# Performance work log

Hardware: AMD Instinct MI355X
Metric: run time of the kernel (lower is better)

Reference implementation:

```python
import jax, jax.numpy as jnp
import numpy as np

N = 100000
E = 1600000
IN_CH = 128
HID = 32
HEADS = 8
OUT_CH = 40
NEG_SLOPE = 0.2


def _glorot(key, shape):
    fan = shape[0] + shape[-1]
    return jax.random.normal(key, shape, dtype=jnp.float32) * jnp.sqrt(2.0 / fan)


def gat_conv(x, src, dst, W, att_src, att_dst, bias, heads, out_ch, concat):
    # PyG GATConv (eval mode, dropout inactive, self-loops already appended)
    n = x.shape[0]
    h = (x @ W).reshape(n, heads, out_ch)              # [N,H,C]
    a_s = jnp.sum(h * att_src, axis=-1)                # [N,H]
    a_d = jnp.sum(h * att_dst, axis=-1)                # [N,H]
    e = jax.nn.leaky_relu(a_s[src] + a_d[dst], NEG_SLOPE)  # [E,H]
    # softmax over incoming edges of each destination node
    m = jax.ops.segment_max(e, dst, num_segments=n)
    e = jnp.exp(e - m[dst])
    denom = jax.ops.segment_sum(e, dst, num_segments=n)
    alpha = e / denom[dst]                              # [E,H]
    msg = h[src] * alpha[:, :, None]                    # [E,H,C] gather + weight
    out = jax.ops.segment_sum(msg, dst, num_segments=n)  # [N,H,C] scatter-add
    if concat:
        out = out.reshape(n, heads * out_ch)
    else:
        out = out.mean(axis=1)
    return out + bias


def setup_inputs() -> dict:
    key = jax.random.key(0)
    ks = jax.random.split(key, 16)
    x = jax.random.normal(ks[0], (N, IN_CH), dtype=jnp.float32)
    edge_index = jax.random.randint(ks[1], (2, E), 0, N, dtype=jnp.int64)
    params = {
        "W1": _glorot(ks[2], (IN_CH, HEADS * HID)),
        "as1": _glorot(ks[3], (HEADS, HID)),
        "ad1": _glorot(ks[4], (HEADS, HID)),
        "b1": jnp.zeros((HEADS * HID,), jnp.float32),
        "W2": _glorot(ks[5], (HEADS * HID, HID)),
        "as2": _glorot(ks[6], (1, HID)),
        "ad2": _glorot(ks[7], (1, HID)),
        "b2": jnp.zeros((HID,), jnp.float32),
        "W3": _glorot(ks[8], (HID, OUT_CH)),
        "as3": _glorot(ks[9], (1, OUT_CH)),
        "ad3": _glorot(ks[10], (1, OUT_CH)),
        "b3": jnp.zeros((OUT_CH,), jnp.float32),
    }
    return {"x": x, "edge_index": edge_index, **params}


def reference(x, edge_index, W1, as1, ad1, b1, W2, as2, ad2, b2, W3, as3, ad3, b3):
    n = x.shape[0]
    # PyG GATConv adds self-loops by default
    loops = jnp.arange(n, dtype=edge_index.dtype)
    src = jnp.concatenate([edge_index[0], loops])
    dst = jnp.concatenate([edge_index[1], loops])

    h = gat_conv(x, src, dst, W1, as1, ad1, b1, HEADS, HID, concat=True)
    h = jax.nn.elu(h)
    h = gat_conv(h, src, dst, W2, as2, ad2, b2, 1, HID, concat=False)
    h = jax.nn.elu(h)
    h = gat_conv(h, src, dst, W3, as3, ad3, b3, 1, OUT_CH, concat=False)
    return jax.nn.log_softmax(h, axis=1)
```

## Files before the change

kernel.cpp:

```cpp
#include <hip/hip_runtime.h>

#define NN 100000
#define NE 1600000
#define ET 1700000
#define NEG 0.2f
#define FNEG 3.4e38f
#define NBSC 98
#define GEMM1_NB 1563
#define PE_NB 6641
#define FATA_NB 8305
#define FILL_CH 425000

#define SRC_OFF   0ULL
#define DST_OFF   6800000ULL
#define RP_OFF    13600000ULL
#define CSR_OFF   14400128ULL
#define W1F_OFF   21200128ULL
#define W2F_OFF   21265664ULL
#define W3F_OFF   21282048ULL
#define SC_OFF    21285120ULL
#define H_OFF     21286144ULL
#define H2B_OFF   72486144ULL
#define H3B_OFF   88486144ULL
#define ALPH_OFF  123686144ULL
#define ASN_OFF   150886144ULL
#define ADN_OFF   154086144ULL
#define AS2_OFF   157286144ULL
#define AD2_OFF   157686144ULL
#define CNT8_OFF  158086144ULL
#define RANK_OFF  161286144ULL
#define WS_NEED   168086144ULL

typedef short bf16x8 __attribute__((ext_vector_type(8)));
typedef float f32x4 __attribute__((ext_vector_type(4)));
typedef float f32x2 __attribute__((ext_vector_type(2)));

__device__ __forceinline__ float lrelu(float x) { return x > 0.f ? x : NEG * x; }
__device__ __forceinline__ float b2f(unsigned short u) {
  return __uint_as_float(((unsigned)u) << 16);
}
__device__ __forceinline__ unsigned short f2bu(float f) {
  unsigned u = __float_as_uint(f);
  return (unsigned short)((u + 0x7FFFu + ((u >> 16) & 1u)) >> 16);
}

__global__ __launch_bounds__(256) void k_sentinel(float* out, int n) {
  int i = blockIdx.x * 256 + threadIdx.x;
  if (i < n) out[i] = 12345.0f;
}

__global__ __launch_bounds__(256) void k_prep_w(const float* __restrict__ W1,
                                                const float* __restrict__ W2,
                                                const float* __restrict__ W3,
                                                unsigned short* __restrict__ W1f,
                                                unsigned short* __restrict__ W2f,
                                                unsigned short* __restrict__ W3f) {
  int idx = blockIdx.x * 256 + threadIdx.x;
  if (idx < 4096) {
    int fg = idx >> 6, lane = idx & 63;
    int mf = fg >> 2, kk = fg & 3;
    int c = mf * 16 + (lane & 15), k0 = kk * 32 + (lane >> 4) * 8;
    unsigned short* o = W1f + idx * 8;
    #pragma unroll
    for (int j = 0; j < 8; ++j) o[j] = f2bu(W1[(k0 + j) * 256 + c]);
  } else if (idx < 5120) {
    int t = idx - 4096;
    int fg = t >> 6, lane = t & 63;
    int mf = fg >> 3, kk = fg & 7;
    int c = mf * 16 + (lane & 15), k0 = kk * 32 + (lane >> 4) * 8;
    unsigned short* o = W2f + t * 8;
    #pragma unroll
    for (int j = 0; j < 8; ++j) o[j] = f2bu(W2[(k0 + j) * 32 + c]);
  } else if (idx < 5312) {
    int t = idx - 5120;
    int mf = t >> 6, lane = t & 63;
    int c = mf * 16 + (lane & 15), k0 = (lane >> 4) * 8;
    unsigned short* o = W3f + t * 8;
    #pragma unroll
    for (int j = 0; j < 8; ++j) o[j] = (c < 40) ? f2bu(W3[(k0 + j) * 40 + c]) : 0;
  }
}

__global__ __launch_bounds__(256) void k_fatA(const int* __restrict__ raw,
                                              int* __restrict__ src,
                                              int* __restrict__ dst,
                                              int* __restrict__ cnt8,
                                              int* __restrict__ rank,
                                              const float* __restrict__ x,
                                              const bf16x8* __restrict__ W1f,
                                              const float* __restrict__ as1,
                                              const float* __restrict__ ad1,
                                              unsigned char* __restrict__ h8,
                                              float* __restrict__ a_s,
                                              float* __restrict__ a_d) {
  __shared__ __align__(16) unsigned short xs[64 * 128];
  __shared__ float asL[256], adL[256];
  const int bid = blockIdx.x;
  const int grp = bid / 5, rem = bid - grp * 5;
  const int tid = threadIdx.x;

  if (rem != 4) {
    int pe = grp * 4 + rem;
    if (pe >= PE_NB) return;
    bool is64 = true;
    #pragma unroll
    for (int i = 1; i < 32; i += 2) is64 = is64 && (raw[i] == 0);
    long long e = (long long)pe * 256 + tid;
    if (e >= ET) return;
    int s, d;
    if (e < NE) {
      if (is64) {
        const long long* r = (const long long*)raw;
        s = (int)r[e];
        d = (int)r[NE + e];
      } else {
        s = raw[e];
        d = raw[NE + e];
      }
    } else {
      s = d = (int)(e - NE);
    }
    src[e] = s;
    dst[e] = d;
    rank[e] = atomicAdd(&cnt8[(tid & 7) * NN + d], 1);
    return;
  }

  if (grp >= GEMM1_NB) return;
  const int n0 = grp * 64;
  asL[tid] = as1[tid];
  adL[tid] = ad1[tid];
  for (int j = tid; j < 2048; j += 256) {
    int r = j >> 5;
    int c4 = (j & 31) << 2;
    long long row = n0 + r; if (row >= NN) row = NN - 1;
    float4 v = *(const float4*)(x + row * 128 + c4);
    unsigned short* p = &xs[r * 128 + c4];
    p[0] = f2bu(v.x); p[1] = f2bu(v.y); p[2] = f2bu(v.z); p[3] = f2bu(v.w);
  }
  __syncthreads();
  const int w = tid >> 6, lane = tid & 63;
  const int nloc = w * 16 + (lane & 15);
  const int node = n0 + nloc;
  bf16x8 bfr[4];
  #pragma unroll
  for (int kk = 0; kk < 4; ++kk)
    bfr[kk] = *(const bf16x8*)&xs[nloc * 128 + kk * 32 + (lane >> 4) * 8];
  const int ch_base = (lane >> 4) * 4;
  float sA[8] = {}, sD[8] = {};
  #pragma unroll
  for (int mf = 0; mf < 16; ++mf) {
    f32x4 acc = {0.f, 0.f, 0.f, 0.f};
    #pragma unroll
    for (int kk = 0; kk < 4; ++kk) {
      bf16x8 af = W1f[(mf * 4 + kk) * 64 + lane];
      acc = __builtin_amdgcn_mfma_f32_16x16x32_bf16(af, bfr[kk], acc, 0, 0, 0);
    }
    const float* av = &asL[mf * 16 + ch_base];
    const float* dv = &adL[mf * 16 + ch_base];
    float ps = acc[0] * av[0] + acc[1] * av[1] + acc[2] * av[2] + acc[3] * av[3];
    float pd = acc[0] * dv[0] + acc[1] * dv[1] + acc[2] * dv[2] + acc[3] * dv[3];
    ps += __shfl_xor(ps, 16); ps += __shfl_xor(ps, 32);
    pd += __shfl_xor(pd, 16); pd += __shfl_xor(pd, 32);
    sA[mf >> 1] += ps; sD[mf >> 1] += pd;
    if (node < NN) {
      int w01 = __builtin_amdgcn_cvt_pk_fp8_f32(acc[0], acc[1], 0, false);
      int w0123 = __builtin_amdgcn_cvt_pk_fp8_f32(acc[2], acc[3], w01, true);
      *(unsigned*)&h8[(unsigned)(node * 256 + mf * 16 + ch_base)] = (unsigned)w0123;
    }
  }
  if (lane < 16 && node < NN) {
    #pragma unroll
    for (int hd = 0; hd < 8; ++hd) {
      a_s[node * 8 + hd] = sA[hd];
      a_d[node * 8 + hd] = sD[hd];
    }
  }
}

__global__ __launch_bounds__(1024) void k_scan_a(int* __restrict__ cnt8,
                                                 int* __restrict__ rowptr,
                                                 int* __restrict__ bsum) {
  __shared__ int wsum[16];
  const int lane = threadIdx.x & 63, wid = threadIdx.x >> 6;
  int i = blockIdx.x * 1024 + threadIdx.x;
  int x = 0;
  if (i < NN) {
    int run = 0;
    #pragma unroll
    for (int k = 0; k < 8; ++k) {
      int c = cnt8[k * NN + i];
      cnt8[k * NN + i] = run;
      run += c;
    }
    x = run;
  }
  int inc = x;
  #pragma unroll
  for (int off = 1; off < 64; off <<= 1) {
    int t = __shfl_up(inc, off);
    if (lane >= off) inc += t;
  }
  if (lane == 63) wsum[wid] = inc;
  __syncthreads();
  if (wid == 0) {
    int w = (lane < 16) ? wsum[lane] : 0;
    #pragma unroll
    for (int off = 1; off < 16; off <<= 1) {
      int t = __shfl_up(w, off);
      if (lane >= off) w += t;
    }
    if (lane < 16) wsum[lane] = w;
  }
  __syncthreads();
  int base = wid ? wsum[wid - 1] : 0;
  if (i < NN) rowptr[i + 1] = base + inc;
  if (threadIdx.x == 1023) bsum[blockIdx.x] = base + inc;
}

__global__ __launch_bounds__(128) void k_scan_b(int* __restrict__ bsum) {
  __shared__ int w0tot;
  int tid = threadIdx.x;
  int v = (tid < NBSC) ? bsum[tid] : 0;
  int inc = v;
  #pragma unroll
  for (int off = 1; off < 64; off <<= 1) {
    int t = __shfl_up(inc, off);
    if ((tid & 63) >= off) inc += t;
  }
  if (tid == 63) w0tot = inc;
  __syncthreads();
  if (tid >= 64) inc += w0tot;
  if (tid < NBSC) bsum[tid] = inc - v;
}

__global__ __launch_bounds__(1024) void k_scan_c(int* __restrict__ rowptr,
                                                 const int* __restrict__ bsum) {
  int i = blockIdx.x * 1024 + threadIdx.x;
  if (i < NN) rowptr[i + 1] += bsum[blockIdx.x];
  if (i == 0) rowptr[0] = 0;
}

__global__ __launch_bounds__(256) void k_fill_nr(const int* __restrict__ src,
                                                 const int* __restrict__ dst,
                                                 const int* __restrict__ rank,
                                                 const int* __restrict__ cnt8,
                                                 const int* __restrict__ rowptr,
                                                 int* __restrict__ csr) {
  int gid = blockIdx.x * 256 + threadIdx.x;
  if (gid >= FILL_CH) return;
  const int h = gid & 7;
  int e0 = gid, e1 = gid + FILL_CH, e2 = gid + 2 * FILL_CH, e3 = gid + 3 * FILL_CH;
  int d0 = dst[e0], d1 = dst[e1], d2 = dst[e2], d3 = dst[e3];
  int r0 = rank[e0], r1 = rank[e1], r2 = rank[e2], r3 = rank[e3];
  int s0 = src[e0], s1 = src[e1], s2 = src[e2], s3 = src[e3];
  int p0 = cnt8[h * NN + d0], p1 = cnt8[h * NN + d1];
  int p2 = cnt8[h * NN + d2], p3 = cnt8[h * NN + d3];
  int b0 = rowptr[d0], b1 = rowptr[d1], b2 = rowptr[d2], b3 = rowptr[d3];
  csr[b0 + p0 + r0] = s0;
  csr[b1 + p1 + r1] = s1;
  csr[b2 + p2 + r2] = s2;
  csr[b3 + p3 + r3] = s3;
}

__global__ __launch_bounds__(256) void k_msalpha1(const int* __restrict__ rowptr,
                                                  const int* __restrict__ csr,
                                                  const float* __restrict__ a_s,
                                                  const float* __restrict__ a_d,
                                                  unsigned short* __restrict__ alph) {
  const int node = blockIdx.x * 4 + (threadIdx.x >> 6);
  const int lane = threadIdx.x & 63;
  const int beg = __builtin_amdgcn_readfirstlane(rowptr[node]);
  const int end = __builtin_amdgcn_readfirstlane(rowptr[node + 1]);
  const int hd = lane & 7;
  const int eg = lane >> 3;
  const float adv = a_d[node * 8 + hd];
  float mx = -FNEG, sm = 0.f;
  if (end - beg <= 32) {
    float vc0 = 0.f, vc1 = 0.f, vc2 = 0.f, vc3 = 0.f;
    #pragma unroll
    for (int k = 0; k < 4; ++k) {
      int i = beg + eg + k * 8;
      if (i < end) {
        float v = lrelu(a_s[csr[i] * 8 + hd] + adv);
        if (k == 0) vc0 = v; else if (k == 1) vc1 = v;
        else if (k == 2) vc2 = v; else vc3 = v;
        float nm = fmaxf(mx, v);
        sm = sm * __expf(mx - nm) + __expf(v - nm);
        mx = nm;
      }
    }
    #pragma unroll
    for (int off = 8; off < 64; off <<= 1) {
      float mo = __shfl_xor(mx, off);
      float so = __shfl_xor(sm, off);
      float nm = fmaxf(mx, mo);
      sm = sm * __expf(mx - nm) + so * __expf(mo - nm);
      mx = nm;
    }
    float rden = 1.0f / sm;
    #pragma unroll
    for (int k = 0; k < 4; ++k) {
      int i = beg + eg + k * 8;
      if (i < end) {
        float v = (k == 0) ? vc0 : (k == 1) ? vc1 : (k == 2) ? vc2 : vc3;
        alph[i * 8 + hd] = f2bu(__expf(v - mx) * rden);
      }
    }
  } else {
    for (int i = beg + eg; i < end; i += 8) {
      int s = csr[i];
      float v = lrelu(a_s[s * 8 + hd] + adv);
      float nm = fmaxf(mx, v);
      sm = sm * __expf(mx - nm) + __expf(v - nm);
      mx = nm;
    }
    #pragma unroll
    for (int off = 8; off < 64; off <<= 1) {
      float mo = __shfl_xor(mx, off);
      float so = __shfl_xor(sm, off);
      float nm = fmaxf(mx, mo);
      sm = sm * __expf(mx - nm) + so * __expf(mo - nm);
      mx = nm;
    }
    float rden = 1.0f / sm;
    for (int i = beg + eg; i < end; i += 8) {
      int s = csr[i];
      float v = lrelu(a_s[s * 8 + hd] + adv);
      alph[i * 8 + hd] = f2bu(__expf(v - mx) * rden);
    }
  }
}

__global__ __launch_bounds__(1024) void k_gather1f(const int* __restrict__ rowptr,
                                                   const int* __restrict__ csr,
                                                   const unsigned short* __restrict__ alph,
                                                   const unsigned char* __restrict__ h8,
                                                   const float* __restrict__ b,
                                                   const bf16x8* __restrict__ W2f,
                                                   const float* __restrict__ as2,
                                                   const float* __restrict__ ad2,
                                                   unsigned short* __restrict__ h2,
                                                   float* __restrict__ a_s,
                                                   float* __restrict__ a_d) {
  __shared__ __align__(16) unsigned short xs[16 * 256];
  const int tid = threadIdx.x;
  const int w = tid >> 6, lane = tid & 63;
  const int n0 = blockIdx.x * 16;
  const int node = n0 + w;
  const int beg = __builtin_amdgcn_readfirstlane(rowptr[node]);
  const int end = __builtin_amdgcn_readfirstlane(rowptr[node + 1]);
  const int hd2 = lane >> 3;
  const unsigned l4 = lane * 4;
  float4 acc = {0.f, 0.f, 0.f, 0.f};
  int i = beg;
  for (; i + 8 <= end; i += 8) {
    int s0 = __builtin_amdgcn_readfirstlane(csr[i]);
    int s1 = __builtin_amdgcn_readfirstlane(csr[i + 1]);
    int s2 = __builtin_amdgcn_readfirstlane(csr[i + 2]);
    int s3 = __builtin_amdgcn_readfirstlane(csr[i + 3]);
    int s4 = __builtin_amdgcn_readfirstlane(csr[i + 4]);
    int s5 = __builtin_amdgcn_readfirstlane(csr[i + 5]);
    int s6 = __builtin_amdgcn_readfirstlane(csr[i + 6]);
    int s7 = __builtin_amdgcn_readfirstlane(csr[i + 7]);
    float a0 = b2f(alph[(i + 0) * 8 + hd2]);
    float a1 = b2f(alph[(i + 1) * 8 + hd2]);
    float a2 = b2f(alph[(i + 2) * 8 + hd2]);
    float a3 = b2f(alph[(i + 3) * 8 + hd2]);
    float a4 = b2f(alph[(i + 4) * 8 + hd2]);
    float a5 = b2f(alph[(i + 5) * 8 + hd2]);
    float a6 = b2f(alph[(i + 6) * 8 + hd2]);
    float a7 = b2f(alph[(i + 7) * 8 + hd2]);
    unsigned w0 = *(const unsigned*)(h8 + ((unsigned)(s0 << 8) + l4));
    unsigned w1 = *(const unsigned*)(h8 + ((unsigned)(s1 << 8) + l4));
    unsigned w2 = *(const unsigned*)(h8 + ((unsigned)(s2 << 8) + l4));
    unsigned w3 = *(const unsigned*)(h8 + ((unsigned)(s3 << 8) + l4));
    unsigned w4 = *(const unsigned*)(h8 + ((unsigned)(s4 << 8) + l4));
    unsigned w5 = *(const unsigned*)(h8 + ((unsigned)(s5 << 8) + l4));
    unsigned w6 = *(const unsigned*)(h8 + ((unsigned)(s6 << 8) + l4));
    unsigned w7 = *(const unsigned*)(h8 + ((unsigned)(s7 << 8) + l4));
    f32x2 lo, hi;
    lo = __builtin_amdgcn_cvt_pk_f32_fp8(w0, false); hi = __builtin_amdgcn_cvt_pk_f32_fp8(w0, true);
    acc.x += a0 * lo[0]; acc.y += a0 * lo[1]; acc.z += a0 * hi[0]; acc.w += a0 * hi[1];
    lo = __builtin_amdgcn_cvt_pk_f32_fp8(w1, false); hi = __builtin_amdgcn_cvt_pk_f32_fp8(w1, true);
    acc.x += a1 * lo[0]; acc.y += a1 * lo[1]; acc.z += a1 * hi[0]; acc.w += a1 * hi[1];
    lo = __builtin_amdgcn_cvt_pk_f32_fp8(w2, false); hi = __builtin_amdgcn_cvt_pk_f32_fp8(w2, true);
    acc.x += a2 * lo[0]; acc.y += a2 * lo[1]; acc.z += a2 * hi[0]; acc.w += a2 * hi[1];
    lo = __builtin_amdgcn_cvt_pk_f32_fp8(w3, false); hi = __builtin_amdgcn_cvt_pk_f32_fp8(w3, true);
    acc.x += a3 * lo[0]; acc.y += a3 * lo[1]; acc.z += a3 * hi[0]; acc.w += a3 * hi[1];
    lo = __builtin_amdgcn_cvt_pk_f32_fp8(w4, false); hi = __builtin_amdgcn_cvt_pk_f32_fp8(w4, true);
    acc.x += a4 * lo[0]; acc.y += a4 * lo[1]; acc.z += a4 * hi[0]; acc.w += a4 * hi[1];
    lo = __builtin_amdgcn_cvt_pk_f32_fp8(w5, false); hi = __builtin_amdgcn_cvt_pk_f32_fp8(w5, true);
    acc.x += a5 * lo[0]; acc.y += a5 * lo[1]; acc.z += a5 * hi[0]; acc.w += a5 * hi[1];
    lo = __builtin_amdgcn_cvt_pk_f32_fp8(w6, false); hi = __builtin_amdgcn_cvt_pk_f32_fp8(w6, true);
    acc.x += a6 * lo[0]; acc.y += a6 * lo[1]; acc.z += a6 * hi[0]; acc.w += a6 * hi[1];
    lo = __builtin_amdgcn_cvt_pk_f32_fp8(w7, false); hi = __builtin_amdgcn_cvt_pk_f32_fp8(w7, true);
    acc.x += a7 * lo[0]; acc.y += a7 * lo[1]; acc.z += a7 * hi[0]; acc.w += a7 * hi[1];
  }
  for (; i < end; ++i) {
    int s0 = __builtin_amdgcn_readfirstlane(csr[i]);
    float a0 = b2f(alph[i * 8 + hd2]);
    unsigned w0 = *(const unsigned*)(h8 + ((unsigned)(s0 << 8) + l4));
    f32x2 lo = __builtin_amdgcn_cvt_pk_f32_fp8(w0, false);
    f32x2 hi = __builtin_amdgcn_cvt_pk_f32_fp8(w0, true);
    acc.x += a0 * lo[0]; acc.y += a0 * lo[1]; acc.z += a0 * hi[0]; acc.w += a0 * hi[1];
  }
  float4 bv = *(const float4*)(b + l4);
  acc.x += bv.x; acc.y += bv.y; acc.z += bv.z; acc.w += bv.w;
  acc.x = acc.x > 0.f ? acc.x : expm1f(acc.x);
  acc.y = acc.y > 0.f ? acc.y : expm1f(acc.y);
  acc.z = acc.z > 0.f ? acc.z : expm1f(acc.z);
  acc.w = acc.w > 0.f ? acc.w : expm1f(acc.w);
  {
    ushort4 o;
    o.x = f2bu(acc.x); o.y = f2bu(acc.y); o.z = f2bu(acc.z); o.w = f2bu(acc.w);
    *(ushort4*)&xs[w * 256 + l4] = o;
  }
  __syncthreads();
  if (w == 0) {
    const int nloc = lane & 15;
    const int node2 = n0 + nloc;
    const int ch_base = (lane >> 4) * 4;
    float sA = 0.f, sD = 0.f;
    #pragma unroll
    for (int mf = 0; mf < 2; ++mf) {
      f32x4 c2 = {0.f, 0.f, 0.f, 0.f};
      #pragma unroll
      for (int kk = 0; kk < 8; ++kk) {
        bf16x8 bfr = *(const bf16x8*)&xs[nloc * 256 + kk * 32 + (lane >> 4) * 8];
        c2 = __builtin_amdgcn_mfma_f32_16x16x32_bf16(W2f[(mf * 8 + kk) * 64 + lane],
                                                     bfr, c2, 0, 0, 0);
      }
      float4 av = *(const float4*)(as2 + mf * 16 + ch_base);
      float4 dv = *(const float4*)(ad2 + mf * 16 + ch_base);
      float ps = c2[0] * av.x + c2[1] * av.y + c2[2] * av.z + c2[3] * av.w;
      float pd = c2[0] * dv.x + c2[1] * dv.y + c2[2] * dv.z + c2[3] * dv.w;
      ps += __shfl_xor(ps, 16); ps += __shfl_xor(ps, 32);
      pd += __shfl_xor(pd, 16); pd += __shfl_xor(pd, 32);
      sA += ps; sD += pd;
      ushort4 o;
      o.x = f2bu(c2[0]); o.y = f2bu(c2[1]); o.z = f2bu(c2[2]); o.w = f2bu(c2[3]);
      *(ushort4*)&h2[(unsigned)(node2 * 32 + mf * 16 + ch_base)] = o;
    }
    if (lane < 16) { a_s[node2] = sA; a_d[node2] = sD; }
  }
}

__global__ __launch_bounds__(512) void k_gather2f(const int* __restrict__ rowptr,
                                                  const int* __restrict__ csr,
                                                  const float* __restrict__ a_s,
                                                  const float* __restrict__ a_d,
                                                  const unsigned short* __restrict__ h,
                                                  const float* __restrict__ b,
                                                  const bf16x8* __restrict__ W3f,
                                                  const float* __restrict__ as3,
                                                  const float* __restrict__ ad3,
                                                  unsigned short* __restrict__ h3,
                                                  float* __restrict__ a_s3,
                                                  float* __restrict__ a_d3) {
  __shared__ __align__(16) unsigned short xs[16 * 32];
  const int tid = threadIdx.x;
  const int hw = tid >> 5, lane32 = tid & 31;
  const int n0 = blockIdx.x * 16;
  const int node = n0 + hw;
  const int beg = rowptr[node], end = rowptr[node + 1];
  const float adv = a_d[node];

  float mx = -FNEG, sm = 0.f;
  for (int i = beg + lane32; i < end; i += 32) {
    float v = lrelu(a_s[csr[i]] + adv);
    float nm = fmaxf(mx, v);
    sm = sm * __expf(mx - nm) + __expf(v - nm);
    mx = nm;
  }
  #pragma unroll
  for (int off = 1; off < 32; off <<= 1) {
    float mo = __shfl_xor(mx, off, 32);
    float so = __shfl_xor(sm, off, 32);
    float nm = fmaxf(mx, mo);
    sm = sm * __expf(mx - nm) + so * __expf(mo - nm);
    mx = nm;
  }
  float rden = 1.0f / sm;

  float acc = 0.f;
  int i = beg;
  for (; i + 4 <= end; i += 4) {
    int s0 = csr[i], s1 = csr[i + 1], s2 = csr[i + 2], s3 = csr[i + 3];
    float a0 = __expf(lrelu(a_s[s0] + adv) - mx) * rden;
    float a1 = __expf(lrelu(a_s[s1] + adv) - mx) * rden;
    float a2 = __expf(lrelu(a_s[s2] + adv) - mx) * rden;
    float a3 = __expf(lrelu(a_s[s3] + adv) - mx) * rden;
    unsigned short v0 = h[(unsigned)(s0 * 32 + lane32)];
    unsigned short v1 = h[(unsigned)(s1 * 32 + lane32)];
    unsigned short v2 = h[(unsigned)(s2 * 32 + lane32)];
    unsigned short v3 = h[(unsigned)(s3 * 32 + lane32)];
    acc += a0 * b2f(v0) + a1 * b2f(v1) + a2 * b2f(v2) + a3 * b2f(v3);
  }
  for (; i < end; ++i) {
    int s0 = csr[i];
    float a0 = __expf(lrelu(a_s[s0] + adv) - mx) * rden;
    acc += a0 * b2f(h[(unsigned)(s0 * 32 + lane32)]);
  }
  acc += b[lane32];
  acc = acc > 0.f ? acc : expm1f(acc);
  xs[hw * 32 + lane32] = f2bu(acc);
  __syncthreads();
  if (tid < 64) {
    const int lane = tid;
    const int nloc = lane & 15;
    const int node3 = n0 + nloc;
    const int ch_base = (lane >> 4) * 4;
    bf16x8 bfr = *(const bf16x8*)&xs[nloc * 32 + (lane >> 4) * 8];
    float sA = 0.f, sD = 0.f;
    #pragma unroll
    for (int mf = 0; mf < 3; ++mf) {
      f32x4 c3 = {0.f, 0.f, 0.f, 0.f};
      c3 = __builtin_amdgcn_mfma_f32_16x16x32_bf16(W3f[mf * 64 + lane], bfr, c3, 0, 0, 0);
      int ch0 = mf * 16 + ch_base;
      float4 av = {0.f, 0.f, 0.f, 0.f}, dv = {0.f, 0.f, 0.f, 0.f};
      if (ch0 < 40) {
        av = *(const float4*)(as3 + ch0);
        dv = *(const float4*)(ad3 + ch0);
      }
      float ps = c3[0] * av.x + c3[1] * av.y + c3[2] * av.z + c3[3] * av.w;
      float pd = c3[0] * dv.x + c3[1] * dv.y + c3[2] * dv.z + c3[3] * dv.w;
      ps += __shfl_xor(ps, 16); ps += __shfl_xor(ps, 32);
      pd += __shfl_xor(pd, 16); pd += __shfl_xor(pd, 32);
      sA += ps; sD += pd;
      if (ch0 < 40) {
        ushort4 o;
        o.x = f2bu(c3[0]); o.y = f2bu(c3[1]); o.z = f2bu(c3[2]); o.w = f2bu(c3[3]);
        *(ushort4*)&h3[(unsigned)(node3 * 40 + ch0)] = o;
      }
    }
    if (lane < 16) { a_s3[node3] = sA; a_d3[node3] = sD; }
  }
}

__global__ __launch_bounds__(256) void k_gather3f(const int* __restrict__ rowptr,
                                                  const int* __restrict__ csr,
                                                  const float* __restrict__ a_s,
                                                  const float* __restrict__ a_d,
                                                  const unsigned short* __restrict__ h,
                                                  const float* __restrict__ b,
                                                  float* __restrict__ out) {
  const int node = blockIdx.x * 4 + (threadIdx.x >> 6);
  const int lane = threadIdx.x & 63;
  const int beg = __builtin_amdgcn_readfirstlane(rowptr[node]);
  const int end = __builtin_amdgcn_readfirstlane(rowptr[node + 1]);
  const float adv = a_d[node];

  float mx = -FNEG, sm = 0.f;
  for (int i = beg + lane; i < end; i += 64) {
    float v = lrelu(a_s[csr[i]] + adv);
    float nm = fmaxf(mx, v);
    sm = sm * __expf(mx - nm) + __expf(v - nm);
    mx = nm;
  }
  #pragma unroll
  for (int off = 1; off < 64; off <<= 1) {
    float mo = __shfl_xor(mx, off);
    float so = __shfl_xor(sm, off);
    float nm = fmaxf(mx, mo);
    sm = sm * __expf(mx - nm) + so * __expf(mo - nm);
    mx = nm;
  }
  float rden = 1.0f / sm;

  float acc = 0.f;
  int i = beg;
  for (; i + 4 <= end; i += 4) {
    int s0 = __builtin_amdgcn_readfirstlane(csr[i]);
    int s1 = __builtin_amdgcn_readfirstlane(csr[i + 1]);
    int s2 = __builtin_amdgcn_readfirstlane(csr[i + 2]);
    int s3 = __builtin_amdgcn_readfirstlane(csr[i + 3]);
    float a0 = __expf(lrelu(a_s[s0] + adv) - mx) * rden;
    float a1 = __expf(lrelu(a_s[s1] + adv) - mx) * rden;
    float a2 = __expf(lrelu(a_s[s2] + adv) - mx) * rden;
    float a3 = __expf(lrelu(a_s[s3] + adv) - mx) * rden;
    if (lane < 40) {
      unsigned short v0 = h[(unsigned)(s0 * 40 + lane)];
      unsigned short v1 = h[(unsigned)(s1 * 40 + lane)];
      unsigned short v2 = h[(unsigned)(s2 * 40 + lane)];
      unsigned short v3 = h[(unsigned)(s3 * 40 + lane)];
      acc += a0 * b2f(v0) + a1 * b2f(v1) + a2 * b2f(v2) + a3 * b2f(v3);
    }
  }
  for (; i < end; ++i) {
    int s0 = __builtin_amdgcn_readfirstlane(csr[i]);
    float a0 = __expf(lrelu(a_s[s0] + adv) - mx) * rden;
    if (lane < 40) acc += a0 * b2f(h[(unsigned)(s0 * 40 + lane)]);
  }
  float v = (lane < 40) ? acc + b[lane] : -FNEG;
  float vmax = v;
  #pragma unroll
  for (int off = 1; off < 64; off <<= 1) vmax = fmaxf(vmax, __shfl_xor(vmax, off));
  float ex = (lane < 40) ? __expf(v - vmax) : 0.f;
  float es = ex;
  #pragma unroll
  for (int off = 1; off < 64; off <<= 1) es += __shfl_xor(es, off);
  float lse = vmax + __logf(es);
  if (lane < 40) out[(long long)node * 40 + lane] = v - lse;
}

extern "C" void kernel_launch(void* const* d_in, const int* in_sizes, int n_in,
                              void* d_out, int out_size, void* d_ws, size_t ws_size,
                              hipStream_t stream) {
  const float* x   = (const float*)d_in[0];
  const int*   eix = (const int*)d_in[1];
  const float* W1  = (const float*)d_in[2];
  const float* as1 = (const float*)d_in[3];
  const float* ad1 = (const float*)d_in[4];
  const float* b1  = (const float*)d_in[5];
  const float* W2  = (const float*)d_in[6];
  const float* as2 = (const float*)d_in[7];
  const float* ad2 = (const float*)d_in[8];
  const float* b2  = (const float*)d_in[9];
  const float* W3  = (const float*)d_in[10];
  const float* as3 = (const float*)d_in[11];
  const float* ad3 = (const float*)d_in[12];
  const float* b3  = (const float*)d_in[13];
  float* out = (float*)d_out;

  if (ws_size < WS_NEED) {
    k_sentinel<<<(out_size + 255) / 256, 256, 0, stream>>>(out, out_size);
    return;
  }

  char* ws = (char*)d_ws;
  int*    src    = (int*)(ws + SRC_OFF);
  int*    dst    = (int*)(ws + DST_OFF);
  int*    rowptr = (int*)(ws + RP_OFF);
  int*    csr    = (int*)(ws + CSR_OFF);
  unsigned short* W1f = (unsigned short*)(ws + W1F_OFF);
  unsigned short* W2f = (unsigned short*)(ws + W2F_OFF);
  unsigned short* W3f = (unsigned short*)(ws + W3F_OFF);
  int*    bsum   = (int*)(ws + SC_OFF);
  unsigned char*  h1q  = (unsigned char*)(ws + H_OFF);
  unsigned short* h2b  = (unsigned short*)(ws + H2B_OFF);
  unsigned short* h3b  = (unsigned short*)(ws + H3B_OFF);
  unsigned short* alph = (unsigned short*)(ws + ALPH_OFF);
  float*  aS     = (float*)(ws + ASN_OFF);
  float*  aD     = (float*)(ws + ADN_OFF);
  float*  aS2    = (float*)(ws + AS2_OFF);
  float*  aD2    = (float*)(ws + AD2_OFF);
  int*    cnt8   = (int*)(ws + CNT8_OFF);
  int*    rank   = (int*)(ws + RANK_OFF);

  hipMemsetAsync(ws + CNT8_OFF, 0, 3200000, stream);
  k_prep_w<<<21, 256, 0, stream>>>(W1, W2, W3, W1f, W2f, W3f);
  k_fatA<<<FATA_NB, 256, 0, stream>>>(eix, src, dst, cnt8, rank, x,
                                      (const bf16x8*)W1f, as1, ad1, h1q, aS, aD);
  k_scan_a<<<NBSC, 1024, 0, stream>>>(cnt8, rowptr, bsum);
  k_scan_b<<<1, 128, 0, stream>>>(bsum);
  k_scan_c<<<NBSC, 1024, 0, stream>>>(rowptr, bsum);
  k_fill_nr<<<(FILL_CH + 255) / 256, 256, 0, stream>>>(src, dst, rank, cnt8,
                                                       rowptr, csr);

  k_msalpha1<<<NN / 4, 256, 0, stream>>>(rowptr, csr, aS, aD, alph);
  k_gather1f<<<NN / 16, 1024, 0, stream>>>(rowptr, csr, alph, h1q, b1,
                                           (const bf16x8*)W2f, as2, ad2,
                                           h2b, aS, aD);

  k_gather2f<<<NN / 16, 512, 0, stream>>>(rowptr, csr, aS, aD, h2b, b2,
                                          (const bf16x8*)W3f, as3, ad3,
                                          h3b, aS2, aD2);

  k_gather3f<<<NN / 4, 256, 0, stream>>>(rowptr, csr, aS2, aD2, h3b, b3, out);
}
```

Before: 394.4 us.

## Fuse layer-1 attention softmax into gather kernel and interleave per-node counters

Removes the separate alpha kernel and its bf16 alpha buffer. The layer-1 gather kernel now computes the per-node, per-head max and sum online from a_s/a_d, then recomputes each alpha inline during aggregation. This avoids one launch plus the write and reread of the alpha array, at the cost of extra exp work and a second pass over the a_s gathers. It also moves the 8-way atomic counters into a node-major layout padded to 16 slots, so one node's counters share a cache line. The attention score buffers are split per layer to avoid aliasing.

```diff
diff --git a/kernel.cpp b/kernel.cpp
--- a/kernel.cpp
+++ b/kernel.cpp
@@ -22,14 +22,15 @@
 #define H_OFF     21286144ULL
 #define H2B_OFF   72486144ULL
 #define H3B_OFF   88486144ULL
-#define ALPH_OFF  123686144ULL
+#define AS3_OFF   123686144ULL
+#define AD3_OFF   124086144ULL
 #define ASN_OFF   150886144ULL
 #define ADN_OFF   154086144ULL
 #define AS2_OFF   157286144ULL
 #define AD2_OFF   157686144ULL
-#define CNT8_OFF  158086144ULL
-#define RANK_OFF  161286144ULL
-#define WS_NEED   168086144ULL
+#define CNT_OFF   158086144ULL
+#define RANK_OFF  164486144ULL
+#define WS_NEED   171286144ULL
 
 typedef short bf16x8 __attribute__((ext_vector_type(8)));
 typedef float f32x4 __attribute__((ext_vector_type(4)));
@@ -84,7 +85,7 @@
 __global__ __launch_bounds__(256) void k_fatA(const int* __restrict__ raw,
                                               int* __restrict__ src,
                                               int* __restrict__ dst,
-                                              int* __restrict__ cnt8,
+                                              int* __restrict__ cnt,
                                               int* __restrict__ rank,
                                               const float* __restrict__ x,
                                               const bf16x8* __restrict__ W1f,
@@ -122,7 +123,7 @@
     }
     src[e] = s;
     dst[e] = d;
-    rank[e] = atomicAdd(&cnt8[(tid & 7) * NN + d], 1);
+    rank[e] = atomicAdd(&cnt[d * 16 + (tid & 7)], 1);
     return;
   }
 
@@ -178,7 +179,7 @@
   }
 }
 
-__global__ __launch_bounds__(1024) void k_scan_a(int* __restrict__ cnt8,
+__global__ __launch_bounds__(1024) void k_scan_a(int* __restrict__ cnt,
                                                  int* __restrict__ rowptr,
                                                  int* __restrict__ bsum) {
   __shared__ int wsum[16];
@@ -189,8 +190,8 @@
     int run = 0;
     #pragma unroll
     for (int k = 0; k < 8; ++k) {
-      int c = cnt8[k * NN + i];
-      cnt8[k * NN + i] = run;
+      int c = cnt[i * 16 + k];
+      cnt[i * 16 + k] = run;
       run += c;
     }
     x = run;
@@ -244,7 +245,7 @@
 __global__ __launch_bounds__(256) void k_fill_nr(const int* __restrict__ src,
                                                  const int* __restrict__ dst,
                                                  const int* __restrict__ rank,
-                                                 const int* __restrict__ cnt8,
+                                                 const int* __restrict__ cnt,
                                                  const int* __restrict__ rowptr,
                                                  int* __restrict__ csr) {
   int gid = blockIdx.x * 256 + threadIdx.x;
@@ -254,8 +255,8 @@
   int d0 = dst[e0], d1 = dst[e1], d2 = dst[e2], d3 = dst[e3];
   int r0 = rank[e0], r1 = rank[e1], r2 = rank[e2], r3 = rank[e3];
   int s0 = src[e0], s1 = src[e1], s2 = src[e2], s3 = src[e3];
-  int p0 = cnt8[h * NN + d0], p1 = cnt8[h * NN + d1];
-  int p2 = cnt8[h * NN + d2], p3 = cnt8[h * NN + d3];
+  int p0 = cnt[d0 * 16 + h], p1 = cnt[d1 * 16 + h];
+  int p2 = cnt[d2 * 16 + h], p3 = cnt[d3 * 16 + h];
   int b0 = rowptr[d0], b1 = rowptr[d1], b2 = rowptr[d2], b3 = rowptr[d3];
   csr[b0 + p0 + r0] = s0;
   csr[b1 + p1 + r1] = s1;
@@ -263,86 +264,18 @@
   csr[b3 + p3 + r3] = s3;
 }
 
-__global__ __launch_bounds__(256) void k_msalpha1(const int* __restrict__ rowptr,
-                                                  const int* __restrict__ csr,
-                                                  const float* __restrict__ a_s,
-                                                  const float* __restrict__ a_d,
-                                                  unsigned short* __restrict__ alph) {
-  const int node = blockIdx.x * 4 + (threadIdx.x >> 6);
-  const int lane = threadIdx.x & 63;
-  const int beg = __builtin_amdgcn_readfirstlane(rowptr[node]);
-  const int end = __builtin_amdgcn_readfirstlane(rowptr[node + 1]);
-  const int hd = lane & 7;
-  const int eg = lane >> 3;
-  const float adv = a_d[node * 8 + hd];
-  float mx = -FNEG, sm = 0.f;
-  if (end - beg <= 32) {
-    float vc0 = 0.f, vc1 = 0.f, vc2 = 0.f, vc3 = 0.f;
-    #pragma unroll
-    for (int k = 0; k < 4; ++k) {
-      int i = beg + eg + k * 8;
-      if (i < end) {
-        float v = lrelu(a_s[csr[i] * 8 + hd] + adv);
-        if (k == 0) vc0 = v; else if (k == 1) vc1 = v;
-        else if (k == 2) vc2 = v; else vc3 = v;
-        float nm = fmaxf(mx, v);
-        sm = sm * __expf(mx - nm) + __expf(v - nm);
-        mx = nm;
-      }
-    }
-    #pragma unroll
-    for (int off = 8; off < 64; off <<= 1) {
-      float mo = __shfl_xor(mx, off);
-      float so = __shfl_xor(sm, off);
-      float nm = fmaxf(mx, mo);
-      sm = sm * __expf(mx - nm) + so * __expf(mo - nm);
-      mx = nm;
-    }
-    float rden = 1.0f / sm;
-    #pragma unroll
-    for (int k = 0; k < 4; ++k) {
-      int i = beg + eg + k * 8;
-      if (i < end) {
-        float v = (k == 0) ? vc0 : (k == 1) ? vc1 : (k == 2) ? vc2 : vc3;
-        alph[i * 8 + hd] = f2bu(__expf(v - mx) * rden);
-      }
-    }
-  } else {
-    for (int i = beg + eg; i < end; i += 8) {
-      int s = csr[i];
-      float v = lrelu(a_s[s * 8 + hd] + adv);
-      float nm = fmaxf(mx, v);
-      sm = sm * __expf(mx - nm) + __expf(v - nm);
-      mx = nm;
-    }
-    #pragma unroll
-    for (int off = 8; off < 64; off <<= 1) {
-      float mo = __shfl_xor(mx, off);
-      float so = __shfl_xor(sm, off);
-      float nm = fmaxf(mx, mo);
-      sm = sm * __expf(mx - nm) + so * __expf(mo - nm);
-      mx = nm;
-    }
-    float rden = 1.0f / sm;
-    for (int i = beg + eg; i < end; i += 8) {
-      int s = csr[i];
-      float v = lrelu(a_s[s * 8 + hd] + adv);
-      alph[i * 8 + hd] = f2bu(__expf(v - mx) * rden);
-    }
-  }
-}
-
 __global__ __launch_bounds__(1024) void k_gather1f(const int* __restrict__ rowptr,
                                                    const int* __restrict__ csr,
-                                                   const unsigned short* __restrict__ alph,
+                                                   const float* __restrict__ as1n,
+                                                   const float* __restrict__ ad1n,
                                                    const unsigned char* __restrict__ h8,
                                                    const float* __restrict__ b,
                                                    const bf16x8* __restrict__ W2f,
                                                    const float* __restrict__ as2,
                                                    const float* __restrict__ ad2,
                                                    unsigned short* __restrict__ h2,
-                                                   float* __restrict__ a_s,
-                                                   float* __restrict__ a_d) {
+                                                   float* __restrict__ a_s2o,
+                                                   float* __restrict__ a_d2o) {
   __shared__ __align__(16) unsigned short xs[16 * 256];
   const int tid = threadIdx.x;
   const int w = tid >> 6, lane = tid & 63;
@@ -350,7 +283,32 @@
   const int node = n0 + w;
   const int beg = __builtin_amdgcn_readfirstlane(rowptr[node]);
   const int end = __builtin_amdgcn_readfirstlane(rowptr[node + 1]);
+
+  {
+  }
+  const int hd = lane & 7;
+  const int eg = lane >> 3;
+  const float adv1 = ad1n[node * 8 + hd];
+  float mx = -FNEG, sm = 0.f;
+  for (int i = beg + eg; i < end; i += 8) {
+    float v = lrelu(as1n[csr[i] * 8 + hd] + adv1);
+    float nm = fmaxf(mx, v);
+    sm = sm * __expf(mx - nm) + __expf(v - nm);
+    mx = nm;
+  }
+  #pragma unroll
+  for (int off = 8; off < 64; off <<= 1) {
+    float mo = __shfl_xor(mx, off);
+    float so = __shfl_xor(sm, off);
+    float nm = fmaxf(mx, mo);
+    sm = sm * __expf(mx - nm) + so * __expf(mo - nm);
+    mx = nm;
+  }
   const int hd2 = lane >> 3;
+  const float m2 = __shfl(mx, hd2);
+  const float rden = 1.0f / __shfl(sm, hd2);
+  const float adv2 = ad1n[node * 8 + hd2];
+
   const unsigned l4 = lane * 4;
   float4 acc = {0.f, 0.f, 0.f, 0.f};
   int i = beg;
@@ -363,14 +321,14 @@
     int s5 = __builtin_amdgcn_readfirstlane(csr[i + 5]);
     int s6 = __builtin_amdgcn_readfirstlane(csr[i + 6]);
     int s7 = __builtin_amdgcn_readfirstlane(csr[i + 7]);
-    float a0 = b2f(alph[(i + 0) * 8 + hd2]);
-    float a1 = b2f(alph[(i + 1) * 8 + hd2]);
-    float a2 = b2f(alph[(i + 2) * 8 + hd2]);
-    float a3 = b2f(alph[(i + 3) * 8 + hd2]);
-    float a4 = b2f(alph[(i + 4) * 8 + hd2]);
-    float a5 = b2f(alph[(i + 5) * 8 + hd2]);
-    float a6 = b2f(alph[(i + 6) * 8 + hd2]);
-    float a7 = b2f(alph[(i + 7) * 8 + hd2]);
+    float u0 = as1n[(unsigned)(s0 * 8) + hd2];
+    float u1 = as1n[(unsigned)(s1 * 8) + hd2];
+    float u2 = as1n[(unsigned)(s2 * 8) + hd2];
+    float u3 = as1n[(unsigned)(s3 * 8) + hd2];
+    float u4 = as1n[(unsigned)(s4 * 8) + hd2];
+    float u5 = as1n[(unsigned)(s5 * 8) + hd2];
+    float u6 = as1n[(unsigned)(s6 * 8) + hd2];
+    float u7 = as1n[(unsigned)(s7 * 8) + hd2];
     unsigned w0 = *(const unsigned*)(h8 + ((unsigned)(s0 << 8) + l4));
     unsigned w1 = *(const unsigned*)(h8 + ((unsigned)(s1 << 8) + l4));
     unsigned w2 = *(const unsigned*)(h8 + ((unsigned)(s2 << 8) + l4));
@@ -379,6 +337,14 @@
     unsigned w5 = *(const unsigned*)(h8 + ((unsigned)(s5 << 8) + l4));
     unsigned w6 = *(const unsigned*)(h8 + ((unsigned)(s6 << 8) + l4));
     unsigned w7 = *(const unsigned*)(h8 + ((unsigned)(s7 << 8) + l4));
+    float a0 = __expf(lrelu(u0 + adv2) - m2) * rden;
+    float a1 = __expf(lrelu(u1 + adv2) - m2) * rden;
+    float a2 = __expf(lrelu(u2 + adv2) - m2) * rden;
+    float a3 = __expf(lrelu(u3 + adv2) - m2) * rden;
+    float a4 = __expf(lrelu(u4 + adv2) - m2) * rden;
+    float a5 = __expf(lrelu(u5 + adv2) - m2) * rden;
+    float a6 = __expf(lrelu(u6 + adv2) - m2) * rden;
+    float a7 = __expf(lrelu(u7 + adv2) - m2) * rden;
     f32x2 lo, hi;
     lo = __builtin_amdgcn_cvt_pk_f32_fp8(w0, false); hi = __builtin_amdgcn_cvt_pk_f32_fp8(w0, true);
     acc.x += a0 * lo[0]; acc.y += a0 * lo[1]; acc.z += a0 * hi[0]; acc.w += a0 * hi[1];
@@ -399,8 +365,9 @@
   }
   for (; i < end; ++i) {
     int s0 = __builtin_amdgcn_readfirstlane(csr[i]);
-    float a0 = b2f(alph[i * 8 + hd2]);
+    float u0 = as1n[(unsigned)(s0 * 8) + hd2];
     unsigned w0 = *(const unsigned*)(h8 + ((unsigned)(s0 << 8) + l4));
+    float a0 = __expf(lrelu(u0 + adv2) - m2) * rden;
     f32x2 lo = __builtin_amdgcn_cvt_pk_f32_fp8(w0, false);
     f32x2 hi = __builtin_amdgcn_cvt_pk_f32_fp8(w0, true);
     acc.x += a0 * lo[0]; acc.y += a0 * lo[1]; acc.z += a0 * hi[0]; acc.w += a0 * hi[1];
@@ -442,7 +409,7 @@
       o.x = f2bu(c2[0]); o.y = f2bu(c2[1]); o.z = f2bu(c2[2]); o.w = f2bu(c2[3]);
       *(ushort4*)&h2[(unsigned)(node2 * 32 + mf * 16 + ch_base)] = o;
     }
-    if (lane < 16) { a_s[node2] = sA; a_d[node2] = sD; }
+    if (lane < 16) { a_s2o[node2] = sA; a_d2o[node2] = sD; }
   }
 }
 
@@ -456,8 +423,8 @@
                                                   const float* __restrict__ as3,
                                                   const float* __restrict__ ad3,
                                                   unsigned short* __restrict__ h3,
-                                                  float* __restrict__ a_s3,
-                                                  float* __restrict__ a_d3) {
+                                                  float* __restrict__ a_s3o,
+                                                  float* __restrict__ a_d3o) {
   __shared__ __align__(16) unsigned short xs[16 * 32];
   const int tid = threadIdx.x;
   const int hw = tid >> 5, lane32 = tid & 31;
@@ -534,7 +501,7 @@
         *(ushort4*)&h3[(unsigned)(node3 * 40 + ch0)] = o;
       }
     }
-    if (lane < 16) { a_s3[node3] = sA; a_d3[node3] = sD; }
+    if (lane < 16) { a_s3o[node3] = sA; a_d3o[node3] = sD; }
   }
 }
 
@@ -640,32 +607,32 @@
   unsigned char*  h1q  = (unsigned char*)(ws + H_OFF);
   unsigned short* h2b  = (unsigned short*)(ws + H2B_OFF);
   unsigned short* h3b  = (unsigned short*)(ws + H3B_OFF);
-  unsigned short* alph = (unsigned short*)(ws + ALPH_OFF);
-  float*  aS     = (float*)(ws + ASN_OFF);
-  float*  aD     = (float*)(ws + ADN_OFF);
+  float*  aS1    = (float*)(ws + ASN_OFF);
+  float*  aD1    = (float*)(ws + ADN_OFF);
   float*  aS2    = (float*)(ws + AS2_OFF);
   float*  aD2    = (float*)(ws + AD2_OFF);
-  int*    cnt8   = (int*)(ws + CNT8_OFF);
+  float*  aS3    = (float*)(ws + AS3_OFF);
+  float*  aD3    = (float*)(ws + AD3_OFF);
+  int*    cnt    = (int*)(ws + CNT_OFF);
   int*    rank   = (int*)(ws + RANK_OFF);
 
-  hipMemsetAsync(ws + CNT8_OFF, 0, 3200000, stream);
+  hipMemsetAsync(ws + CNT_OFF, 0, 6400000, stream);
   k_prep_w<<<21, 256, 0, stream>>>(W1, W2, W3, W1f, W2f, W3f);
-  k_fatA<<<FATA_NB, 256, 0, stream>>>(eix, src, dst, cnt8, rank, x,
-                                      (const bf16x8*)W1f, as1, ad1, h1q, aS, aD);
-  k_scan_a<<<NBSC, 1024, 0, stream>>>(cnt8, rowptr, bsum);
+  k_fatA<<<FATA_NB, 256, 0, stream>>>(eix, src, dst, cnt, rank, x,
+                                      (const bf16x8*)W1f, as1, ad1, h1q, aS1, aD1);
+  k_scan_a<<<NBSC, 1024, 0, stream>>>(cnt, rowptr, bsum);
   k_scan_b<<<1, 128, 0, stream>>>(bsum);
   k_scan_c<<<NBSC, 1024, 0, stream>>>(rowptr, bsum);
-  k_fill_nr<<<(FILL_CH + 255) / 256, 256, 0, stream>>>(src, dst, rank, cnt8,
+  k_fill_nr<<<(FILL_CH + 255) / 256, 256, 0, stream>>>(src, dst, rank, cnt,
                                                        rowptr, csr);
 
-  k_msalpha1<<<NN / 4, 256, 0, stream>>>(rowptr, csr, aS, aD, alph);
-  k_gather1f<<<NN / 16, 1024, 0, stream>>>(rowptr, csr, alph, h1q, b1,
+  k_gather1f<<<NN / 16, 1024, 0, stream>>>(rowptr, csr, aS1, aD1, h1q, b1,
                                            (const bf16x8*)W2f, as2, ad2,
-                                           h2b, aS, aD);
-
-  k_gather2f<<<NN / 16, 512, 0, stream>>>(rowptr, csr, aS, aD, h2b, b2,
+                                           h2b, aS2, aD2);
+
+  k_gather2f<<<NN / 16, 512, 0, stream>>>(rowptr, csr, aS2, aD2, h2b, b2,
                                           (const bf16x8*)W3f, as3, ad3,
-                                          h3b, aS2, aD2);
-
-  k_gather3f<<<NN / 4, 256, 0, stream>>>(rowptr, csr, aS2, aD2, h3b, b3, out);
-}
+                                          h3b, aS3, aD3);
+
+  k_gather3f<<<NN / 4, 256, 0, stream>>>(rowptr, csr, aS3, aD3, h3b, b3, out);
+}
```

Result: no change. 400.0 us (+1.4%).
